# Optimization experiments

Measured on AMD Instinct MI355X. Metric: run time of the kernel, lower is better.

Reference implementation:

```python
import jax, jax.numpy as jnp
import numpy as np

USER_NUM = 50000
ITEM_NUM = 50000
N = USER_NUM + ITEM_NUM
VT_DIM = 512
CAT_NUM = 1000
CAT_DIM = 32
HIDDEN = 128
OUT = 64
E = 2_000_000
BAG = 5


def setup_inputs() -> dict:
    key = jax.random.key(0)
    ks = jax.random.split(key, 12)
    inp = {
        "vt_feature": jax.random.normal(ks[0], (ITEM_NUM, VT_DIM), jnp.float32),
        "cat_indices": jax.random.randint(ks[1], (ITEM_NUM * BAG,), 0, CAT_NUM),
        "cat_offsets": jnp.arange(ITEM_NUM) * BAG,
        "edge_index": jax.random.randint(ks[2], (2, E), 0, N),
        # learned parameters
        "cat_table": jax.random.normal(ks[3], (CAT_NUM, CAT_DIM), jnp.float32) * 0.1,
        "fuse_w": jax.random.normal(ks[4], (HIDDEN, VT_DIM + CAT_DIM), jnp.float32) * (1.0 / np.sqrt(VT_DIM + CAT_DIM)),
        "user": jax.random.normal(ks[5], (USER_NUM, HIDDEN), jnp.float32) * 0.1,
        "w1_l": jax.random.normal(ks[6], (HIDDEN, HIDDEN), jnp.float32) * (1.0 / np.sqrt(HIDDEN)),
        "b1": jnp.zeros((HIDDEN,), jnp.float32),
        "w1_r": jax.random.normal(ks[7], (HIDDEN, HIDDEN), jnp.float32) * (1.0 / np.sqrt(HIDDEN)),
        "w2_l": jax.random.normal(ks[8], (OUT, HIDDEN), jnp.float32) * (1.0 / np.sqrt(HIDDEN)),
        "b2": jnp.zeros((OUT,), jnp.float32),
        "w2_r": jax.random.normal(ks[9], (OUT, HIDDEN), jnp.float32) * (1.0 / np.sqrt(HIDDEN)),
    }
    return inp


def _embedding_bag_mean(table, indices, offsets, num_bags):
    # EmbeddingBag(mode='mean') with offsets: segment-mean of table lookups.
    pos = jnp.arange(indices.shape[0])
    seg = jnp.searchsorted(offsets, pos, side="right") - 1  # bag id per index
    sums = jax.ops.segment_sum(table[indices], seg, num_segments=num_bags)
    cnt = jax.ops.segment_sum(jnp.ones_like(pos, jnp.float32), seg, num_segments=num_bags)
    return sums / jnp.maximum(cnt, 1.0)[:, None]


def _sage_conv(x, edge_index, w_l, b_l, w_r):
    # PyG SAGEConv (aggr='mean'): lin_l(mean_{j->i} x_j) + lin_r(x_i)
    src, dst = edge_index[0], edge_index[1]
    agg = jax.ops.segment_sum(x[src], dst, num_segments=N)
    deg = jax.ops.segment_sum(jnp.ones((src.shape[0],), x.dtype), dst, num_segments=N)
    agg = agg / jnp.maximum(deg, 1.0)[:, None]
    return agg @ w_l.T + b_l + x @ w_r.T


def reference(vt_feature, cat_indices, cat_offsets, edge_index, cat_table,
              fuse_w, user, w1_l, b1, w1_r, w2_l, b2, w2_r):
    cat_emb = _embedding_bag_mean(cat_table, cat_indices, cat_offsets, ITEM_NUM)
    item_feat = jnp.concatenate([vt_feature, cat_emb], axis=1) @ fuse_w.T
    x0 = jnp.concatenate([user, item_feat], axis=0)  # [N, hidden]
    x1 = jax.nn.leaky_relu(_sage_conv(x0, edge_index, w1_l, b1, w1_r), negative_slope=0.01)
    # dropout is identity in eval mode
    x2 = _sage_conv(x1, edge_index, w2_l, b2, w2_r)
    return x2
```

## Files before the change

### kernel.cpp

```cpp
#include <hip/hip_runtime.h>

#define USER_N   50000
#define ITEM_N   50000
#define NNODE    100000
#define VT_DIM   512
#define CAT_DIM  32
#define HIDDEN   128
#define OUTD     64
#define PADCAP   64

#define BINC    8192
#define NBKT    98
#define BSHIFT  10
#define SLICES  8
#define BKT_CAP 24576

#define AGG_BLOCKS 4096

typedef __attribute__((ext_vector_type(8))) short short8;
typedef __attribute__((ext_vector_type(4))) float f32x4;

__device__ __forceinline__ float bf2f(unsigned short u) {
    return __uint_as_float(((unsigned int)u) << 16);
}
__device__ __forceinline__ unsigned short f2bf(float f) {
    unsigned int u = __float_as_uint(f);
    unsigned int r = u + 0x7fffu + ((u >> 16) & 1u);
    return (unsigned short)(r >> 16);
}
__device__ __forceinline__ unsigned int pk2(float lo, float hi) {
    return ((unsigned int)f2bf(hi) << 16) | (unsigned int)f2bf(lo);
}
__device__ __forceinline__ void acc8w(float* a, uint4 v, float w) {
    a[0] += w * __uint_as_float(v.x << 16);
    a[1] += w * __uint_as_float(v.x & 0xffff0000u);
    a[2] += w * __uint_as_float(v.y << 16);
    a[3] += w * __uint_as_float(v.y & 0xffff0000u);
    a[4] += w * __uint_as_float(v.z << 16);
    a[5] += w * __uint_as_float(v.z & 0xffff0000u);
    a[6] += w * __uint_as_float(v.w << 16);
    a[7] += w * __uint_as_float(v.w & 0xffff0000u);
}

__global__ __launch_bounds__(256) void k_copy_user(const float* __restrict__ user,
                                                   unsigned short* __restrict__ x0, int n4) {
    int gid = blockIdx.x * 256 + threadIdx.x;
    if (gid >= n4) return;
    float4 v = ((const float4*)user)[gid];
    ushort4 o;
    o.x = f2bf(v.x); o.y = f2bf(v.y); o.z = f2bf(v.z); o.w = f2bf(v.w);
    ((ushort4*)x0)[gid] = o;
}

#define ASTR 40
#define XSTR 136

__global__ __launch_bounds__(256, 4) void k_fuse_mfma(const float* __restrict__ vt,
                                                      const float* __restrict__ cat_table,
                                                      const int* __restrict__ cat_idx,
                                                      const int* __restrict__ cat_off,
                                                      const float* __restrict__ fw,
                                                      unsigned short* __restrict__ x0,
                                                      int total_idx) {
    __shared__ __align__(16) unsigned short Al[64 * ASTR];
    __shared__ __align__(16) unsigned short Bl[128 * ASTR];
    __shared__ __align__(16) unsigned short Cl[64 * CAT_DIM];
    int tid = threadIdx.x;
    int wave = tid >> 6, lane = tid & 63, quad = lane >> 4, l16 = lane & 15;
    int br0 = blockIdx.x * 64;
    int row = tid >> 2, q4 = tid & 3;
    int arow = br0 + row;

#pragma unroll
    for (int i = 0; i < 8; i++) {
        int idx = tid + i * 256;
        int it = idx >> 5, d = idx & 31;
        int item = br0 + it;
        float acc = 0.f;
        int cnt = 1;
        if (item < ITEM_N) {
            int s = cat_off[item];
            int e = (item + 1 < ITEM_N) ? cat_off[item + 1] : total_idx;
            cnt = e - s;
            for (int j = s; j < e; ++j) acc += cat_table[cat_idx[j] * CAT_DIM + d];
        }
        float inv = 1.f / (float)(cnt > 0 ? cnt : 1);
        Cl[it * CAT_DIM + d] = (item < ITEM_N) ? f2bf(acc * inv) : (unsigned short)0;
    }

    f32x4 acc[8];
#pragma unroll
    for (int n = 0; n < 8; n++) acc[n] = (f32x4){0.f, 0.f, 0.f, 0.f};

    for (int kb = 0; kb < 17; ++kb) {
        if (kb < 16) {
            if (arow < ITEM_N) {
                const float* src = vt + (size_t)arow * VT_DIM + kb * 32 + q4 * 8;
                float4 v0 = ((const float4*)src)[0];
                float4 v1 = ((const float4*)src)[1];
                ushort4 o0, o1;
                o0.x = f2bf(v0.x); o0.y = f2bf(v0.y); o0.z = f2bf(v0.z); o0.w = f2bf(v0.w);
                o1.x = f2bf(v1.x); o1.y = f2bf(v1.y); o1.z = f2bf(v1.z); o1.w = f2bf(v1.w);
                *(ushort4*)&Al[row * ASTR + q4 * 8]     = o0;
                *(ushort4*)&Al[row * ASTR + q4 * 8 + 4] = o1;
            } else {
                ushort4 z = {0, 0, 0, 0};
                *(ushort4*)&Al[row * ASTR + q4 * 8]     = z;
                *(ushort4*)&Al[row * ASTR + q4 * 8 + 4] = z;
            }
        }
        {
            int n = tid & 127, kh = tid >> 7;
            const float* src = fw + (size_t)n * (VT_DIM + CAT_DIM) + kb * 32 + kh * 16;
#pragma unroll
            for (int i = 0; i < 4; i++) {
                float4 v = ((const float4*)src)[i];
                ushort4 o;
                o.x = f2bf(v.x); o.y = f2bf(v.y); o.z = f2bf(v.z); o.w = f2bf(v.w);
                *(ushort4*)&Bl[n * ASTR + kh * 16 + i * 4] = o;
            }
        }
        __syncthreads();
        short8 av = (kb < 16)
            ? *(const short8*)&Al[(wave * 16 + l16) * ASTR + quad * 8]
            : *(const short8*)&Cl[(wave * 16 + l16) * CAT_DIM + quad * 8];
#pragma unroll
        for (int nf = 0; nf < 8; nf++) {
            short8 bv = *(const short8*)&Bl[(nf * 16 + l16) * ASTR + quad * 8];
            acc[nf] = __builtin_amdgcn_mfma_f32_16x16x32_bf16(av, bv, acc[nf], 0, 0, 0);
        }
        __syncthreads();
    }
    int rbase = br0 + wave * 16 + quad * 4;
#pragma unroll
    for (int r = 0; r < 4; r++) {
        int orow = rbase + r;
        if (orow < ITEM_N) {
#pragma unroll
            for (int nf = 0; nf < 8; nf++) {
                int col = nf * 16 + l16;
                x0[(size_t)(USER_N + orow) * HIDDEN + col] = f2bf(acc[nf][r]);
            }
        }
    }
}

__global__ __launch_bounds__(256, 4) void k_l12_mfma(const unsigned short* __restrict__ agg1,
                                                     const unsigned short* __restrict__ x0,
                                                     const float* __restrict__ w1l,
                                                     const float* __restrict__ w1r,
                                                     const float* __restrict__ b1,
                                                     const float* __restrict__ w2l,
                                                     const float* __restrict__ w2r,
                                                     const float* __restrict__ b2,
                                                     unsigned short* __restrict__ y1,
                                                     float* __restrict__ outw) {
    __shared__ __align__(16) unsigned short Al[64 * ASTR];
    __shared__ __align__(16) unsigned short Bl[128 * ASTR];
    __shared__ __align__(16) unsigned short Xl[64 * XSTR];
    int tid = threadIdx.x;
    int wave = tid >> 6, lane = tid & 63, quad = lane >> 4, l16 = lane & 15;
    int br0 = blockIdx.x * 64;
    int row = tid >> 2, q4 = tid & 3;
    int arow = br0 + row;

    f32x4 acc[8];
#pragma unroll
    for (int n = 0; n < 8; n++) acc[n] = (f32x4){0.f, 0.f, 0.f, 0.f};

    for (int kb = 0; kb < 8; ++kb) {
        const unsigned short* abase = (kb < 4) ? agg1 : x0;
        int kc = (kb & 3) * 32;
        if (arow < NNODE) {
            uint4 v = *(const uint4*)(abase + (size_t)arow * HIDDEN + kc + q4 * 8);
            *(uint4*)&Al[row * ASTR + q4 * 8] = v;
        } else {
            uint4 z = {0, 0, 0, 0};
            *(uint4*)&Al[row * ASTR + q4 * 8] = z;
        }
        {
            int n = tid & 127, kh = tid >> 7;
            const float* src = ((kb < 4) ? w1l : w1r) + (size_t)n * HIDDEN + kc + kh * 16;
#pragma unroll
            for (int i = 0; i < 4; i++) {
                float4 v = ((const float4*)src)[i];
                ushort4 o;
                o.x = f2bf(v.x); o.y = f2bf(v.y); o.z = f2bf(v.z); o.w = f2bf(v.w);
                *(ushort4*)&Bl[n * ASTR + kh * 16 + i * 4] = o;
            }
        }
        __syncthreads();
        short8 av = *(const short8*)&Al[(wave * 16 + l16) * ASTR + quad * 8];
#pragma unroll
        for (int nf = 0; nf < 8; nf++) {
            short8 bv = *(const short8*)&Bl[(nf * 16 + l16) * ASTR + quad * 8];
            acc[nf] = __builtin_amdgcn_mfma_f32_16x16x32_bf16(av, bv, acc[nf], 0, 0, 0);
        }
        __syncthreads();
    }
    {
        float bias[8];
#pragma unroll
        for (int nf = 0; nf < 8; nf++) bias[nf] = b1[nf * 16 + l16];
        int lr0 = wave * 16 + quad * 4;
#pragma unroll
        for (int r = 0; r < 4; r++) {
#pragma unroll
            for (int nf = 0; nf < 8; nf++) {
                float v = acc[nf][r] + bias[nf];
                v = (v >= 0.f) ? v : 0.01f * v;
                Xl[(lr0 + r) * XSTR + nf * 16 + l16] = f2bf(v);
            }
        }
    }
    __syncthreads();

#pragma unroll
    for (int n = 0; n < 8; n++) acc[n] = (f32x4){0.f, 0.f, 0.f, 0.f};
    for (int kb = 0; kb < 4; ++kb) {
        int kc = kb * 32;
        {
            int n = tid & 127, kh = tid >> 7;
            const float* wsrc = (n < 64) ? (w2l + (size_t)n * HIDDEN)
                                         : (w2r + (size_t)(n - 64) * HIDDEN);
            const float* src = wsrc + kc + kh * 16;
#pragma unroll
            for (int i = 0; i < 4; i++) {
                float4 v = ((const float4*)src)[i];
                ushort4 o;
                o.x = f2bf(v.x); o.y = f2bf(v.y); o.z = f2bf(v.z); o.w = f2bf(v.w);
                *(ushort4*)&Bl[n * ASTR + kh * 16 + i * 4] = o;
            }
        }
        __syncthreads();
        short8 av = *(const short8*)&Xl[(wave * 16 + l16) * XSTR + kc + quad * 8];
#pragma unroll
        for (int nf = 0; nf < 8; nf++) {
            short8 bv = *(const short8*)&Bl[(nf * 16 + l16) * ASTR + quad * 8];
            acc[nf] = __builtin_amdgcn_mfma_f32_16x16x32_bf16(av, bv, acc[nf], 0, 0, 0);
        }
        __syncthreads();
    }
    float bias2[4];
#pragma unroll
    for (int nf = 0; nf < 4; nf++) bias2[nf] = b2[nf * 16 + l16];
    int rbase = br0 + wave * 16 + quad * 4;
#pragma unroll
    for (int r = 0; r < 4; r++) {
        int orow = rbase + r;
        if (orow < NNODE) {
#pragma unroll
            for (int nf = 0; nf < 4; nf++) {
                int col = nf * 16 + l16;
                y1[(size_t)orow * OUTD + col] = f2bf(acc[nf][r]);
            }
#pragma unroll
            for (int nf = 4; nf < 8; nf++) {
                int col = (nf - 4) * 16 + l16;
                outw[(size_t)orow * OUTD + col] = acc[nf][r] + bias2[nf - 4];
            }
        }
    }
}

__global__ __launch_bounds__(256) void k_deg(const int* __restrict__ dst, int ne4, int ne, int* __restrict__ deg) {
    int t = blockIdx.x * 256 + threadIdx.x;
    int base = t * 4;
    if (t < ne4) {
        int4 d4 = *(const int4*)&dst[base];
        atomicAdd(&deg[d4.x], 1);
        atomicAdd(&deg[d4.y], 1);
        atomicAdd(&deg[d4.z], 1);
        atomicAdd(&deg[d4.w], 1);
    } else {
        for (int e = base; e < ne; ++e) atomicAdd(&deg[dst[e]], 1);
    }
}

__global__ __launch_bounds__(256) void k_scanA(const int* __restrict__ deg, int n, int* __restrict__ bsum) {
    __shared__ int sd[256];
    int i = blockIdx.x * 256 + threadIdx.x;
    sd[threadIdx.x] = (i < n) ? deg[i] : 0;
    __syncthreads();
    for (int o = 128; o > 0; o >>= 1) {
        if (threadIdx.x < o) sd[threadIdx.x] += sd[threadIdx.x + o];
        __syncthreads();
    }
    if (threadIdx.x == 0) bsum[blockIdx.x] = sd[0];
}

__global__ __launch_bounds__(512) void k_scanB(const int* __restrict__ bsum, int nb, int* __restrict__ boff) {
    __shared__ int sd[512];
    int t = threadIdx.x;
    int v = (t < nb) ? bsum[t] : 0;
    sd[t] = v;
    __syncthreads();
    for (int o = 1; o < 512; o <<= 1) {
        int x = 0;
        if (t >= o) x = sd[t - o];
        __syncthreads();
        sd[t] += x;
        __syncthreads();
    }
    if (t < nb) boff[t] = sd[t] - v;
}

__global__ __launch_bounds__(256) void k_scanC(const int* __restrict__ deg, int n,
                                               const int* __restrict__ boff,
                                               int* __restrict__ offs, int* __restrict__ cursor, int ne) {
    __shared__ int sd[256];
    int i = blockIdx.x * 256 + threadIdx.x;
    int v = (i < n) ? deg[i] : 0;
    sd[threadIdx.x] = v;
    __syncthreads();
    for (int o = 1; o < 256; o <<= 1) {
        int x = 0;
        if (threadIdx.x >= o) x = sd[threadIdx.x - o];
        __syncthreads();
        sd[threadIdx.x] += x;
        __syncthreads();
    }
    if (i < n) {
        int ex = boff[blockIdx.x] + sd[threadIdx.x] - v;
        offs[i] = ex;
        cursor[i] = ex;
    }
    if (i == 0) offs[n] = ne;
}

__global__ __launch_bounds__(256) void k_scatter(const int* __restrict__ src, const int* __restrict__ dst,
                                                 int ne4, int ne, int* __restrict__ cursor, int* __restrict__ csr) {
    int t = blockIdx.x * 256 + threadIdx.x;
    int base = t * 4;
    if (t < ne4) {
        int4 d4 = *(const int4*)&dst[base];
        int4 s4 = *(const int4*)&src[base];
        int p0 = atomicAdd(&cursor[d4.x], 1);
        int p1 = atomicAdd(&cursor[d4.y], 1);
        int p2 = atomicAdd(&cursor[d4.z], 1);
        int p3 = atomicAdd(&cursor[d4.w], 1);
        csr[p0] = s4.x;
        csr[p1] = s4.y;
        csr[p2] = s4.z;
        csr[p3] = s4.w;
    } else {
        for (int e = base; e < ne; ++e) {
            int slot = atomicAdd(&cursor[dst[e]], 1);
            csr[slot] = src[e];
        }
    }
}

__global__ __launch_bounds__(256) void k_binscatter_f(const int* __restrict__ src,
                                                      const int* __restrict__ dst,
                                                      int ne,
                                                      int* __restrict__ bktcnt,
                                                      int2* __restrict__ ebin) {
    __shared__ int lh[NBKT];
    int b = blockIdx.x;
    for (int i = threadIdx.x; i < NBKT; i += 256) lh[i] = 0;
    __syncthreads();
    int s = b * BINC;
    int e = (s + BINC < ne) ? (s + BINC) : ne;
    int nv = (e - s) & ~3;
    for (int j = s + threadIdx.x * 4; j < s + nv; j += 1024) {
        int4 d4 = *(const int4*)&dst[j];
        atomicAdd(&lh[d4.x >> BSHIFT], 1);
        atomicAdd(&lh[d4.y >> BSHIFT], 1);
        atomicAdd(&lh[d4.z >> BSHIFT], 1);
        atomicAdd(&lh[d4.w >> BSHIFT], 1);
    }
    for (int j = s + nv + threadIdx.x; j < e; j += 256) {
        atomicAdd(&lh[dst[j] >> BSHIFT], 1);
    }
    __syncthreads();
    for (int i = threadIdx.x; i < NBKT; i += 256) lh[i] = atomicAdd(&bktcnt[i], lh[i]);
    __syncthreads();
    for (int j = s + threadIdx.x * 4; j < s + nv; j += 1024) {
        int4 d4 = *(const int4*)&dst[j];
        int4 s4 = *(const int4*)&src[j];
        int b0 = d4.x >> BSHIFT, b1_ = d4.y >> BSHIFT, b2_ = d4.z >> BSHIFT, b3 = d4.w >> BSHIFT;
        int p0 = atomicAdd(&lh[b0], 1);
        int p1 = atomicAdd(&lh[b1_], 1);
        int p2 = atomicAdd(&lh[b2_], 1);
        int p3 = atomicAdd(&lh[b3], 1);
        if (p0 < BKT_CAP) ebin[(size_t)b0 * BKT_CAP + p0] = make_int2(s4.x, d4.x);
        if (p1 < BKT_CAP) ebin[(size_t)b1_ * BKT_CAP + p1] = make_int2(s4.y, d4.y);
        if (p2 < BKT_CAP) ebin[(size_t)b2_ * BKT_CAP + p2] = make_int2(s4.z, d4.z);
        if (p3 < BKT_CAP) ebin[(size_t)b3 * BKT_CAP + p3] = make_int2(s4.w, d4.w);
    }
    for (int j = s + nv + threadIdx.x; j < e; j += 256) {
        int d = dst[j];
        int b0 = d >> BSHIFT;
        int p = atomicAdd(&lh[b0], 1);
        if (p < BKT_CAP) ebin[(size_t)b0 * BKT_CAP + p] = make_int2(src[j], d);
    }
}

__global__ __launch_bounds__(256) void k_scatter_bkt(const int2* __restrict__ ebin,
                                                     const int* __restrict__ bktcnt,
                                                     int* __restrict__ cursor,
                                                     int* __restrict__ csrp) {
    int xcd = blockIdx.x & 7;
    int w = blockIdx.x >> 3;
    int i = w / SLICES, sl = w - i * SLICES;
    int b = xcd + (i << 3);
    if (b >= NBKT) return;
    int len = bktcnt[b];
    if (len > BKT_CAP) len = BKT_CAP;
    int s0 = b * BKT_CAP;
    int e0 = s0 + len;
    int per = (len + SLICES - 1) / SLICES;
    int s = s0 + sl * per;
    int e = (s + per < e0) ? (s + per) : e0;
    for (int j = s + threadIdx.x; j < e; j += 256) {
        int2 p = ebin[j];
        int slot = atomicAdd(&cursor[p.y], 1);
        if (slot < PADCAP) csrp[p.y * PADCAP + slot] = p.x;
    }
}

__global__ __launch_bounds__(256) void k_agg1(const unsigned short* __restrict__ x0,
                                              const int* __restrict__ offs,
                                              const int* __restrict__ cnts,
                                              int pad,
                                              const int* __restrict__ csr,
                                              unsigned short* __restrict__ agg1) {
    int lane = threadIdx.x & 63;
    int quad = lane >> 4;
    int l16 = lane & 15;
    int wstride = gridDim.x << 2;
    for (int wid = (blockIdx.x << 2) + (threadIdx.x >> 6); wid < NNODE; wid += wstride) {
        int s, e, d;
        if (pad) {
            s = wid << 6;
            int c = cnts[wid];
            d = c;
            e = s + (c < PADCAP ? c : PADCAP);
        } else {
            s = offs[wid];
            e = offs[wid + 1];
            d = e - s;
        }
        float a[8];
#pragma unroll
        for (int i = 0; i < 8; i++) a[i] = 0.f;
        for (int j = s; j < e; j += 32) {
            int sn[8];
            float w[8];
#pragma unroll
            for (int t = 0; t < 8; t++) {
                int myj = j + 4 * t + quad;
                bool ok = (myj < e);
                sn[t] = ok ? csr[myj] : csr[s];
                w[t] = ok ? 1.f : 0.f;
            }
            uint4 v[8];
#pragma unroll
            for (int t = 0; t < 8; t++)
                v[t] = *(const uint4*)&x0[(size_t)sn[t] * HIDDEN + l16 * 8];
#pragma unroll
            for (int t = 0; t < 8; t++) acc8w(a, v[t], w[t]);
        }
#pragma unroll
        for (int i = 0; i < 8; i++) {
            a[i] += __shfl_xor(a[i], 16, 64);
            a[i] += __shfl_xor(a[i], 32, 64);
        }
        float inv = 1.f / (float)(d > 0 ? d : 1);
        if (quad == 0) {
            uint4 o;
            o.x = pk2(a[0] * inv, a[1] * inv);
            o.y = pk2(a[2] * inv, a[3] * inv);
            o.z = pk2(a[4] * inv, a[5] * inv);
            o.w = pk2(a[6] * inv, a[7] * inv);
            *(uint4*)&agg1[(size_t)wid * HIDDEN + l16 * 8] = o;
        }
    }
}

__global__ __launch_bounds__(256) void k_agg2_out(const unsigned short* __restrict__ y1,
                                                  const int* __restrict__ offs,
                                                  const int* __restrict__ cnts,
                                                  int pad,
                                                  const int* __restrict__ csr,
                                                  float* __restrict__ out) {
    int lane = threadIdx.x & 63;
    int oct = lane >> 3;
    int l8 = lane & 7;
    int wstride = gridDim.x << 2;
    for (int wid = (blockIdx.x << 2) + (threadIdx.x >> 6); wid < NNODE; wid += wstride) {
        int s, e, d;
        if (pad) {
            s = wid << 6;
            int c = cnts[wid];
            d = c;
            e = s + (c < PADCAP ? c : PADCAP);
        } else {
            s = offs[wid];
            e = offs[wid + 1];
            d = e - s;
        }
        float a[8];
#pragma unroll
        for (int i = 0; i < 8; i++) a[i] = 0.f;
        for (int j = s; j < e; j += 64) {
            int sn[8];
            float w[8];
#pragma unroll
            for (int t = 0; t < 8; t++) {
                int myj = j + 8 * t + oct;
                bool ok = (myj < e);
                sn[t] = ok ? csr[myj] : csr[s];
                w[t] = ok ? 1.f : 0.f;
            }
            uint4 v[8];
#pragma unroll
            for (int t = 0; t < 8; t++)
                v[t] = *(const uint4*)&y1[(size_t)sn[t] * OUTD + l8 * 8];
#pragma unroll
            for (int t = 0; t < 8; t++) acc8w(a, v[t], w[t]);
        }
#pragma unroll
        for (int i = 0; i < 8; i++) {
            a[i] += __shfl_xor(a[i], 8, 64);
            a[i] += __shfl_xor(a[i], 16, 64);
            a[i] += __shfl_xor(a[i], 32, 64);
        }
        float inv = 1.f / (float)(d > 0 ? d : 1);
        if (oct == 0) {
            float4* op = (float4*)&out[(size_t)wid * OUTD + l8 * 8];
            float4 p0 = op[0];
            float4 p1 = op[1];
            float4 o0, o1;
            o0.x = a[0] * inv + p0.x; o0.y = a[1] * inv + p0.y;
            o0.z = a[2] * inv + p0.z; o0.w = a[3] * inv + p0.w;
            o1.x = a[4] * inv + p1.x; o1.y = a[5] * inv + p1.y;
            o1.z = a[6] * inv + p1.z; o1.w = a[7] * inv + p1.w;
            op[0] = o0;
            op[1] = o1;
        }
    }
}

extern "C" void kernel_launch(void* const* d_in, const int* in_sizes, int n_in,
                              void* d_out, int out_size, void* d_ws, size_t ws_size,
                              hipStream_t stream) {
    const float* vt      = (const float*)d_in[0];
    const int*   cat_idx = (const int*)d_in[1];
    const int*   cat_off = (const int*)d_in[2];
    const int*   ei      = (const int*)d_in[3];
    const float* cat_tab = (const float*)d_in[4];
    const float* fuse_w  = (const float*)d_in[5];
    const float* user    = (const float*)d_in[6];
    const float* w1l     = (const float*)d_in[7];
    const float* b1      = (const float*)d_in[8];
    const float* w1r     = (const float*)d_in[9];
    const float* w2l     = (const float*)d_in[10];
    const float* b2      = (const float*)d_in[11];
    const float* w2r     = (const float*)d_in[12];
    float* out = (float*)d_out;

    const int ne = in_sizes[3] / 2;
    const int ne4 = ne / 4;
    const int total_idx = in_sizes[1];
    const int* esrc = ei;
    const int* edst = ei + ne;

    const size_t SZ_X0  = (size_t)NNODE * HIDDEN * 2;
    const size_t SZ_PAD = (size_t)NNODE * PADCAP * 4;
    const size_t SZ_CSR = (size_t)ne * 4;
    const size_t SZ_INT = (size_t)NNODE * 4;
    const size_t SZ_EBIN = (size_t)NBKT * BKT_CAP * 8;

    size_t need_pad = SZ_X0 * 2 + (SZ_EBIN > SZ_X0 ? SZ_EBIN : SZ_X0) + SZ_PAD + SZ_INT + 8192;
    size_t need_csr = SZ_X0 * 3 + SZ_CSR + SZ_INT * 3 + 4 * 4096 + 4096;

    char* p = (char*)d_ws;
    auto alloc = [&](size_t bytes) {
        char* q = p;
        p += (bytes + 255) & ~(size_t)255;
        return q;
    };

    const int nscan = (NNODE + 255) / 256;
    const int sc_blocks = (ne4 + 255) / 256;
    const int nblk = (ne + BINC - 1) / BINC;

    if (ws_size >= need_pad) {
        unsigned short* x0   = (unsigned short*)alloc(SZ_X0);
        unsigned short* aggY = (unsigned short*)alloc(SZ_X0);
        char*           SCR  = (char*)alloc(SZ_EBIN > SZ_X0 ? SZ_EBIN : SZ_X0);
        int*            csrp = (int*)alloc(SZ_PAD);
        int*          cursor = (int*)alloc(SZ_INT + 1024);
        int*          bktcnt = cursor + NNODE;

        int2*           ebin = (int2*)SCR;
        unsigned short* y1   = (unsigned short*)SCR;

        k_copy_user<<<(USER_N * HIDDEN / 4 + 255) / 256, 256, 0, stream>>>(user, x0, USER_N * HIDDEN / 4);
        k_fuse_mfma<<<(ITEM_N + 63) / 64, 256, 0, stream>>>(vt, cat_tab, cat_idx, cat_off, fuse_w, x0, total_idx);

        hipMemsetAsync(cursor, 0, SZ_INT + 1024, stream);
        k_binscatter_f<<<nblk, 256, 0, stream>>>(esrc, edst, ne, bktcnt, ebin);
        k_scatter_bkt<<<8 * 13 * SLICES, 256, 0, stream>>>(ebin, bktcnt, cursor, csrp);

        k_agg1<<<AGG_BLOCKS, 256, 0, stream>>>(x0, cursor, cursor, 1, csrp, aggY);
        k_l12_mfma<<<(NNODE + 63) / 64, 256, 0, stream>>>(aggY, x0, w1l, w1r, b1, w2l, w2r, b2, y1, out);
        k_agg2_out<<<AGG_BLOCKS, 256, 0, stream>>>(y1, cursor, cursor, 1, csrp, out);
    } else if (ws_size >= need_csr) {
        unsigned short* x0   = (unsigned short*)alloc(SZ_X0);
        unsigned short* aggY = (unsigned short*)alloc(SZ_X0);
        unsigned short* y1   = (unsigned short*)alloc(SZ_X0);
        char*           R4   = (char*)alloc(SZ_CSR);
        int* deg    = (int*)alloc(SZ_INT);
        int* offs   = (int*)alloc(SZ_INT + 256);
        int* cursor = (int*)alloc(SZ_INT);
        int* bsum   = (int*)alloc(512 * 4);
        int* boff   = (int*)alloc(512 * 4);
        int* csr    = (int*)R4;

        k_copy_user<<<(USER_N * HIDDEN / 4 + 255) / 256, 256, 0, stream>>>(user, x0, USER_N * HIDDEN / 4);
        k_fuse_mfma<<<(ITEM_N + 63) / 64, 256, 0, stream>>>(vt, cat_tab, cat_idx, cat_off, fuse_w, x0, total_idx);

        hipMemsetAsync(deg, 0, SZ_INT, stream);
        k_deg<<<sc_blocks, 256, 0, stream>>>(edst, ne4, ne, deg);
        k_scanA<<<nscan, 256, 0, stream>>>(deg, NNODE, bsum);
        k_scanB<<<1, 512, 0, stream>>>(bsum, nscan, boff);
        k_scanC<<<nscan, 256, 0, stream>>>(deg, NNODE, boff, offs, cursor, ne);
        k_scatter<<<sc_blocks, 256, 0, stream>>>(esrc, edst, ne4, ne, cursor, csr);

        k_agg1<<<AGG_BLOCKS, 256, 0, stream>>>(x0, offs, offs, 0, csr, aggY);
        k_l12_mfma<<<(NNODE + 63) / 64, 256, 0, stream>>>(aggY, x0, w1l, w1r, b1, w2l, w2r, b2, y1, out);
        k_agg2_out<<<AGG_BLOCKS, 256, 0, stream>>>(y1, offs, offs, 0, csr, out);
    } else {
        hipMemsetAsync(d_out, 0, (size_t)out_size * 4, stream);
    }
}
```

Baseline: 503.2 us.

## Stage full fuse weight in LDS once per block and stream A directly to registers

The fuse GEMM kernel now launches 256 blocks of 1024 threads. Each block converts the whole 128x544 fuse weight to bf16 in LDS once, then each wave handles a 16-row item tile and loads vt rows straight from global memory into MFMA operand registers. This removes the per-k-step A/B LDS staging and the repeated syncthreads, and it stops re-converting the weight for every 64-row tile. In exchange it uses about 141KB of LDS, allowing one block per CU, and each lane's vt loads are less coalesced. The category bag-mean is also computed per lane with vectorized loads directly into the A fragment.

```diff
diff --git a/kernel.cpp b/kernel.cpp
--- a/kernel.cpp
+++ b/kernel.cpp
@@ -30,6 +30,12 @@
 }
 __device__ __forceinline__ unsigned int pk2(float lo, float hi) {
     return ((unsigned int)f2bf(hi) << 16) | (unsigned int)f2bf(lo);
+}
+__device__ __forceinline__ short8 cvt8(float4 a, float4 b) {
+    union { unsigned short u[8]; short8 s; } r;
+    r.u[0] = f2bf(a.x); r.u[1] = f2bf(a.y); r.u[2] = f2bf(a.z); r.u[3] = f2bf(a.w);
+    r.u[4] = f2bf(b.x); r.u[5] = f2bf(b.y); r.u[6] = f2bf(b.z); r.u[7] = f2bf(b.w);
+    return r.s;
 }
 __device__ __forceinline__ void acc8w(float* a, uint4 v, float w) {
     a[0] += w * __uint_as_float(v.x << 16);
@@ -54,84 +60,79 @@
 
 #define ASTR 40
 #define XSTR 136
-
-__global__ __launch_bounds__(256, 4) void k_fuse_mfma(const float* __restrict__ vt,
-                                                      const float* __restrict__ cat_table,
-                                                      const int* __restrict__ cat_idx,
-                                                      const int* __restrict__ cat_off,
-                                                      const float* __restrict__ fw,
-                                                      unsigned short* __restrict__ x0,
-                                                      int total_idx) {
-    __shared__ __align__(16) unsigned short Al[64 * ASTR];
-    __shared__ __align__(16) unsigned short Bl[128 * ASTR];
-    __shared__ __align__(16) unsigned short Cl[64 * CAT_DIM];
+#define BSTR 552
+
+__global__ __launch_bounds__(1024, 1) void k_fuse_mfma(const float* __restrict__ vt,
+                                                       const float* __restrict__ cat_table,
+                                                       const int* __restrict__ cat_idx,
+                                                       const int* __restrict__ cat_off,
+                                                       const float* __restrict__ fw,
+                                                       unsigned short* __restrict__ x0,
+                                                       int total_idx) {
+    __shared__ __align__(16) unsigned short Bl[128 * BSTR];
     int tid = threadIdx.x;
+
+#pragma unroll
+    for (int i = 0; i < 17; i++) {
+        int idx = tid + i * 1024;
+        int col = idx / 136;
+        int k4 = idx - col * 136;
+        float4 v = *(const float4*)(fw + (size_t)col * (VT_DIM + CAT_DIM) + k4 * 4);
+        ushort4 o;
+        o.x = f2bf(v.x); o.y = f2bf(v.y); o.z = f2bf(v.z); o.w = f2bf(v.w);
+        *(ushort4*)&Bl[col * BSTR + k4 * 4] = o;
+    }
+    __syncthreads();
+
     int wave = tid >> 6, lane = tid & 63, quad = lane >> 4, l16 = lane & 15;
-    int br0 = blockIdx.x * 64;
-    int row = tid >> 2, q4 = tid & 3;
-    int arow = br0 + row;
-
-#pragma unroll
-    for (int i = 0; i < 8; i++) {
-        int idx = tid + i * 256;
-        int it = idx >> 5, d = idx & 31;
-        int item = br0 + it;
-        float acc = 0.f;
-        int cnt = 1;
-        if (item < ITEM_N) {
-            int s = cat_off[item];
-            int e = (item + 1 < ITEM_N) ? cat_off[item + 1] : total_idx;
-            cnt = e - s;
-            for (int j = s; j < e; ++j) acc += cat_table[cat_idx[j] * CAT_DIM + d];
-        }
+    int t = blockIdx.x + (wave << 8);
+    if (t >= (ITEM_N + 15) / 16) return;
+    int r0 = t * 16;
+
+    short8 cav;
+    {
+        int item = r0 + l16;
+        int s = cat_off[item];
+        int e = (item + 1 < ITEM_N) ? cat_off[item + 1] : total_idx;
+        float a[8];
+#pragma unroll
+        for (int i = 0; i < 8; i++) a[i] = 0.f;
+        for (int j = s; j < e; ++j) {
+            const float* cr = cat_table + (size_t)cat_idx[j] * CAT_DIM + quad * 8;
+            float4 c0 = ((const float4*)cr)[0];
+            float4 c1 = ((const float4*)cr)[1];
+            a[0] += c0.x; a[1] += c0.y; a[2] += c0.z; a[3] += c0.w;
+            a[4] += c1.x; a[5] += c1.y; a[6] += c1.z; a[7] += c1.w;
+        }
+        int cnt = e - s;
         float inv = 1.f / (float)(cnt > 0 ? cnt : 1);
-        Cl[it * CAT_DIM + d] = (item < ITEM_N) ? f2bf(acc * inv) : (unsigned short)0;
+        float4 f0 = {a[0] * inv, a[1] * inv, a[2] * inv, a[3] * inv};
+        float4 f1 = {a[4] * inv, a[5] * inv, a[6] * inv, a[7] * inv};
+        cav = cvt8(f0, f1);
     }
 
     f32x4 acc[8];
 #pragma unroll
     for (int n = 0; n < 8; n++) acc[n] = (f32x4){0.f, 0.f, 0.f, 0.f};
 
+    const float* vrow = vt + (size_t)(r0 + l16) * VT_DIM + quad * 8;
     for (int kb = 0; kb < 17; ++kb) {
+        short8 av;
         if (kb < 16) {
-            if (arow < ITEM_N) {
-                const float* src = vt + (size_t)arow * VT_DIM + kb * 32 + q4 * 8;
-                float4 v0 = ((const float4*)src)[0];
-                float4 v1 = ((const float4*)src)[1];
-                ushort4 o0, o1;
-                o0.x = f2bf(v0.x); o0.y = f2bf(v0.y); o0.z = f2bf(v0.z); o0.w = f2bf(v0.w);
-                o1.x = f2bf(v1.x); o1.y = f2bf(v1.y); o1.z = f2bf(v1.z); o1.w = f2bf(v1.w);
-                *(ushort4*)&Al[row * ASTR + q4 * 8]     = o0;
-                *(ushort4*)&Al[row * ASTR + q4 * 8 + 4] = o1;
-            } else {
-                ushort4 z = {0, 0, 0, 0};
-                *(ushort4*)&Al[row * ASTR + q4 * 8]     = z;
-                *(ushort4*)&Al[row * ASTR + q4 * 8 + 4] = z;
-            }
-        }
-        {
-            int n = tid & 127, kh = tid >> 7;
-            const float* src = fw + (size_t)n * (VT_DIM + CAT_DIM) + kb * 32 + kh * 16;
-#pragma unroll
-            for (int i = 0; i < 4; i++) {
-                float4 v = ((const float4*)src)[i];
-                ushort4 o;
-                o.x = f2bf(v.x); o.y = f2bf(v.y); o.z = f2bf(v.z); o.w = f2bf(v.w);
-                *(ushort4*)&Bl[n * ASTR + kh * 16 + i * 4] = o;
-            }
-        }
-        __syncthreads();
-        short8 av = (kb < 16)
-            ? *(const short8*)&Al[(wave * 16 + l16) * ASTR + quad * 8]
-            : *(const short8*)&Cl[(wave * 16 + l16) * CAT_DIM + quad * 8];
+            float4 v0 = *(const float4*)(vrow + kb * 32);
+            float4 v1 = *(const float4*)(vrow + kb * 32 + 4);
+            av = cvt8(v0, v1);
+        } else {
+            av = cav;
+        }
 #pragma unroll
         for (int nf = 0; nf < 8; nf++) {
-            short8 bv = *(const short8*)&Bl[(nf * 16 + l16) * ASTR + quad * 8];
+            short8 bv = *(const short8*)&Bl[(nf * 16 + l16) * BSTR + kb * 32 + quad * 8];
             acc[nf] = __builtin_amdgcn_mfma_f32_16x16x32_bf16(av, bv, acc[nf], 0, 0, 0);
         }
-        __syncthreads();
-    }
-    int rbase = br0 + wave * 16 + quad * 4;
+    }
+
+    int rbase = r0 + quad * 4;
 #pragma unroll
     for (int r = 0; r < 4; r++) {
         int orow = rbase + r;
@@ -599,7 +600,7 @@
         unsigned short* y1   = (unsigned short*)SCR;
 
         k_copy_user<<<(USER_N * HIDDEN / 4 + 255) / 256, 256, 0, stream>>>(user, x0, USER_N * HIDDEN / 4);
-        k_fuse_mfma<<<(ITEM_N + 63) / 64, 256, 0, stream>>>(vt, cat_tab, cat_idx, cat_off, fuse_w, x0, total_idx);
+        k_fuse_mfma<<<256, 1024, 0, stream>>>(vt, cat_tab, cat_idx, cat_off, fuse_w, x0, total_idx);
 
         hipMemsetAsync(cursor, 0, SZ_INT + 1024, stream);
         k_binscatter_f<<<nblk, 256, 0, stream>>>(esrc, edst, ne, bktcnt, ebin);
@@ -621,7 +622,7 @@
         int* csr    = (int*)R4;
 
         k_copy_user<<<(USER_N * HIDDEN / 4 + 255) / 256, 256, 0, stream>>>(user, x0, USER_N * HIDDEN / 4);
-        k_fuse_mfma<<<(ITEM_N + 63) / 64, 256, 0, stream>>>(vt, cat_tab, cat_idx, cat_off, fuse_w, x0, total_idx);
+        k_fuse_mfma<<<256, 1024, 0, stream>>>(vt, cat_tab, cat_idx, cat_off, fuse_w, x0, total_idx);
 
         hipMemsetAsync(deg, 0, SZ_INT, stream);
         k_deg<<<sc_blocks, 256, 0, stream>>>(edst, ne4, ne, deg);
```

Result: faster. 470.3 us (-6.5%).
